# Kernel tuning notes

Hardware: AMD Instinct MI355X
Metric: run time of the kernel (lower is better)

## Reference

```python
import jax, jax.numpy as jnp
import numpy as np

NMS_PRE_MAXSIZE = 4096
NMS_POST_MAXSIZE = 512
NMS_THRESH = 0.7


def setup_inputs() -> dict:
    key = jax.random.key(0)
    k1, k2, k3, k4, k5 = jax.random.split(key, 5)
    B, N, C = 4, 32768, 3
    # realistic 3D boxes: (x, y, z, dx, dy, dz, heading)
    xy = jax.random.uniform(k1, (B, N, 2), dtype=jnp.float32) * 70.0
    z = jax.random.uniform(k2, (B, N, 1), dtype=jnp.float32) * 4.0 - 2.0
    sizes = jax.random.uniform(k3, (B, N, 3), dtype=jnp.float32) * 3.0 + 1.0
    heading = jax.random.uniform(k4, (B, N, 1), dtype=jnp.float32) * 6.2832 - 3.1416
    batch_box_preds = jnp.concatenate([xy, z, sizes, heading], axis=-1)  # (B,N,7)
    batch_cls_preds = jax.random.uniform(k5, (B, N, C), dtype=jnp.float32)  # (B,N,3)
    return {"batch_box_preds": batch_box_preds, "batch_cls_preds": batch_cls_preds}


def _nms_single(boxes, scores, labels):
    # boxes (N,7), scores (N,), labels (N,) int32
    top_s, idx = jax.lax.top_k(scores, NMS_PRE_MAXSIZE)   # sort desc, keep pre-maxsize
    b = boxes[idx]                                        # (PRE,7)
    l = labels[idx]
    # BEV axis-aligned IoU (reference surrogate for the rotated-BEV CUDA IoU kernel)
    x, y, dx, dy = b[:, 0], b[:, 1], b[:, 3], b[:, 4]
    x1, x2 = x - 0.5 * dx, x + 0.5 * dx
    y1, y2 = y - 0.5 * dy, y + 0.5 * dy
    area = dx * dy
    ix = jnp.maximum(0.0, jnp.minimum(x2[:, None], x2[None, :]) - jnp.maximum(x1[:, None], x1[None, :]))
    iy = jnp.maximum(0.0, jnp.minimum(y2[:, None], y2[None, :]) - jnp.maximum(y1[:, None], y1[None, :]))
    inter = ix * iy
    iou = jax.lax.stop_gradient(inter / (area[:, None] + area[None, :] - inter + 1e-6))

    ar = jnp.arange(NMS_PRE_MAXSIZE)

    def body(i, keep):
        sup = (iou[i] > NMS_THRESH) & (ar > i) & keep[i]
        return keep & ~sup

    keep = jax.lax.fori_loop(0, NMS_PRE_MAXSIZE, body, jnp.ones(NMS_PRE_MAXSIZE, bool))

    # pack first NMS_POST_MAXSIZE kept boxes into fixed-size zero-padded outputs
    rank = jnp.cumsum(keep) - 1
    valid = keep & (rank < NMS_POST_MAXSIZE)
    pos = jnp.where(valid, rank, NMS_POST_MAXSIZE)  # invalid -> scratch row
    rois = jnp.zeros((NMS_POST_MAXSIZE + 1, 7), b.dtype).at[pos].set(b)[:NMS_POST_MAXSIZE]
    sc = jnp.zeros((NMS_POST_MAXSIZE + 1,), top_s.dtype).at[pos].set(top_s)[:NMS_POST_MAXSIZE]
    lb = jnp.zeros((NMS_POST_MAXSIZE + 1,), jnp.int32).at[pos].set(l)[:NMS_POST_MAXSIZE]
    return rois, sc, lb


def reference(batch_box_preds, batch_cls_preds):
    # per-box max score / argmax class (torch.max(cls_preds, dim=1) per sample)
    roi_scores_all = jnp.max(batch_cls_preds, axis=-1)                 # (B,N)
    roi_labels_all = jnp.argmax(batch_cls_preds, axis=-1).astype(jnp.int32)
    rois, roi_scores, roi_labels = jax.vmap(_nms_single)(batch_box_preds, roi_scores_all, roi_labels_all)
    return rois, roi_scores, roi_labels + 1  # labels shifted by +1 as in proposal_layer
```

## Files before the change

kernel.cpp:

```cpp
#include <hip/hip_runtime.h>
#include <stdint.h>

#define BB 4
#define NN 32768
#define PRE 4096
#define POST 512
#define NMS_TH 0.7f
#define MIDCAP 8192
#define P1G 16

typedef unsigned long long u64;
typedef unsigned int u32;

__device__ __forceinline__ u32 orderable(float f) {
  u32 u = __float_as_uint(f);
  return (u & 0x80000000u) ? ~u : (u | 0x80000000u);
}
__device__ __forceinline__ float unorderable(u32 o) {
  u32 u = (o & 0x80000000u) ? (o & 0x7fffffffu) : ~o;
  return __uint_as_float(u);
}
__device__ __forceinline__ u32 bucket_of(float s) {
  u32 v = (u32)(s * 2147483648.0f);
  u32 bk = v >> 20;
  return bk > 2047u ? 2047u : bk;
}
__device__ __forceinline__ u64 readlane64(u64 v, int l) {
  u32 lo = (u32)__builtin_amdgcn_readlane((int)(u32)v, l);
  u32 hi = (u32)__builtin_amdgcn_readlane((int)(u32)(v >> 32), l);
  return ((u64)hi << 32) | lo;
}

__global__ void zero_kernel(u32* __restrict__ hist, u32* __restrict__ cnt_mid,
                            u64* __restrict__ rowAnyBm) {
  int t = blockIdx.x * 256 + threadIdx.x;
  if (t < BB * 2048) hist[t] = 0;
  if (t < BB * 64) rowAnyBm[t] = 0;
  if (t < BB) cnt_mid[t] = 0;
}

__global__ __launch_bounds__(256) void score_hist_kernel(const float* __restrict__ cls,
                                                         int* __restrict__ labels,
                                                         u64* __restrict__ keys,
                                                         u32* __restrict__ hist) {
  __shared__ u32 lh[2048];
  for (int t = threadIdx.x; t < 2048; t += 256) lh[t] = 0;
  __syncthreads();
  int g = blockIdx.x * 256 + threadIdx.x;
  const float* c = cls + (size_t)g * 3;
  float s = c[0]; int l = 0;
  float c1 = c[1], c2 = c[2];
  if (c1 > s) { s = c1; l = 1; }
  if (c2 > s) { s = c2; l = 2; }
  int n = g & (NN - 1);
  keys[g] = ((u64)orderable(s) << 32) | (u32)(~(u32)n);
  labels[g] = l;
  atomicAdd(&lh[bucket_of(s)], 1u);
  __syncthreads();
  int b = blockIdx.x >> 7;
  for (int t = threadIdx.x; t < 2048; t += 256) {
    u32 v = lh[t];
    if (v) atomicAdd(&hist[b * 2048 + t], v);
  }
}

__global__ __launch_bounds__(256) void select_kernel(const u32* __restrict__ hist,
                                                     u32* __restrict__ selinfo,
                                                     u32* __restrict__ sfxBuf,
                                                     u32* __restrict__ cursor) {
  __shared__ u32 sfx[2048];
  int b = blockIdx.x;
  for (int t = threadIdx.x; t < 2048; t += 256) sfx[t] = hist[b * 2048 + t];
  __syncthreads();
  for (int d = 1; d < 2048; d <<= 1) {
    u32 v[8];
#pragma unroll
    for (int i = 0; i < 8; ++i) {
      int t = threadIdx.x + i * 256;
      v[i] = (t + d < 2048) ? sfx[t + d] : 0;
    }
    __syncthreads();
#pragma unroll
    for (int i = 0; i < 8; ++i) sfx[threadIdx.x + i * 256] += v[i];
    __syncthreads();
  }
  for (int t = threadIdx.x; t < 2048; t += 256) {
    u32 above = (t + 1 < 2048) ? sfx[t + 1] : 0;
    sfxBuf[b * 2048 + t] = sfx[t];
    cursor[b * 2048 + t] = above;
    if (above < PRE && sfx[t] >= PRE) { selinfo[b * 2] = (u32)t; selinfo[b * 2 + 1] = above; }
  }
}

__global__ __launch_bounds__(256) void compact_kernel(const u64* __restrict__ keys,
                                                      const u32* __restrict__ selinfo,
                                                      u32* __restrict__ cursor,
                                                      u64* __restrict__ sel, u64* __restrict__ mid,
                                                      u32* __restrict__ cnt_mid) {
  int g = blockIdx.x * 256 + threadIdx.x;
  int b = g >> 15;
  u64 key = keys[g];
  u32 bk = bucket_of(unorderable((u32)(key >> 32)));
  u32 T = selinfo[b * 2];
  if (bk > T) {
    u32 p = atomicAdd(&cursor[b * 2048 + bk], 1u);
    sel[((size_t)b << 12) + p] = key;
  } else if (bk == T) {
    u32 p = atomicAdd(&cnt_mid[b], 1u);
    if (p < MIDCAP) mid[(size_t)b * MIDCAP + p] = key;
  }
}

__global__ __launch_bounds__(64) void bsort_kernel(u64* __restrict__ sel, u64* __restrict__ mid,
                                                   const u32* __restrict__ sfxBuf,
                                                   const u32* __restrict__ selinfo,
                                                   const u32* __restrict__ cnt_mid,
                                                   const float* __restrict__ boxes,
                                                   const int* __restrict__ labels,
                                                   float* __restrict__ topBox,
                                                   float4* __restrict__ P,
                                                   float* __restrict__ AR,
                                                   float* __restrict__ topS,
                                                   int* __restrict__ topL) {
  int t = blockIdx.x & 2047;
  int b = blockIdx.x >> 11;
  int lane = threadIdx.x;
  u32 T = selinfo[b * 2];
  if ((u32)t < T) return;
  u64* selB = sel + ((size_t)b << 12);
  u32 start, end;
  if ((u32)t == T) {
    u32 C1 = selinfo[b * 2 + 1];
    int need = PRE - (int)C1;
    int M = (int)cnt_mid[b]; if (M > MIDCAP) M = MIDCAP;
    u64* midB = mid + (size_t)b * MIDCAP;
    for (int r = 0; r < need; ++r) {
      u64 best = 0; int bi = -1;
      for (int q = lane; q < M; q += 64) {
        u64 v = midB[q];
        if (v > best) { best = v; bi = q; }
      }
#pragma unroll
      for (int d = 32; d > 0; d >>= 1) {
        u64 ob = __shfl_xor(best, d, 64);
        int oi = __shfl_xor(bi, d, 64);
        if (ob > best) { best = ob; bi = oi; }
      }
      if (lane == 0) selB[C1 + r] = best;
      if (bi >= 0 && lane == (bi & 63)) midB[bi] = 0;
    }
    start = C1; end = PRE;
  } else {
    start = (t < 2047) ? sfxBuf[b * 2048 + t + 1] : 0u;
    end = sfxBuf[b * 2048 + t];
    int n = (int)(end - start);
    if (n > 64) {
      for (int r = 0; r < n - 1; ++r) {
        u64 best = 0; int bi = -1;
        for (int q = r + lane; q < n; q += 64) {
          u64 v = selB[start + q];
          if (v > best) { best = v; bi = q; }
        }
#pragma unroll
        for (int d = 32; d > 0; d >>= 1) {
          u64 ob = __shfl_xor(best, d, 64);
          int oi = __shfl_xor(bi, d, 64);
          if (ob > best) { best = ob; bi = oi; }
        }
        if (lane == 0) {
          u64 tmp = selB[start + r];
          selB[start + r] = best;
          selB[start + bi] = tmp;
        }
      }
    } else if (n > 1) {
      u64 v = (lane < n) ? selB[start + lane] : 0ULL;
#pragma unroll
      for (int k = 2; k <= 64; k <<= 1) {
#pragma unroll
        for (int j = k >> 1; j > 0; j >>= 1) {
          u64 o = __shfl_xor(v, j, 64);
          bool up = ((lane & k) == 0);
          bool first = ((lane & j) == 0);
          u64 mx = v > o ? v : o, mn = v > o ? o : v;
          v = (first == up) ? mx : mn;
        }
      }
      if (lane < n) selB[start + lane] = v;
    }
  }
  __builtin_amdgcn_s_waitcnt(0);
  for (u32 pos = start + lane; pos < end; pos += 64) {
    u64 key = selB[pos];
    u32 n = ~(u32)key;
    size_t src = (size_t)b * NN + n;
    const float* bx = boxes + src * 7;
    float x = bx[0], y = bx[1], dx = bx[3], dy = bx[4];
    size_t gidx = ((size_t)b << 12) + pos;
    float* tb = topBox + gidx * 7;
#pragma unroll
    for (int c = 0; c < 7; ++c) tb[c] = bx[c];
    float4 p;
    p.x = x - 0.5f * dx; p.z = x + 0.5f * dx;
    p.y = y - 0.5f * dy; p.w = y + 0.5f * dy;
    P[gidx] = p;
    AR[gidx] = dx * dy;
    topS[gidx] = unorderable((u32)(key >> 32));
    topL[gidx] = labels[src];
  }
}

__device__ __forceinline__ void mask_tile(int b, int rb, int w, int lane,
                                          const float4* __restrict__ P,
                                          const float* __restrict__ AR,
                                          u64* __restrict__ maskT,
                                          u64* __restrict__ diag,
                                          u64* __restrict__ rowAnyBm) {
  int base = b << 12;
  int row = (rb << 6) + lane;
  float4 rp = P[base + row];
  float rar = AR[base + row];
  const float4* __restrict__ Pcol = P + base + (w << 6);
  const float* __restrict__ ARcol = AR + base + (w << 6);
  u64 bits = 0;
  float margMin = 1.0f;
#pragma unroll 8
  for (int k = 0; k < 64; ++k) {
    float4 cb = Pcol[k];
    float ca = ARcol[k];
    float ix = fminf(rp.z, cb.z) - fmaxf(rp.x, cb.x); ix = fmaxf(0.0f, ix);
    float iy = fminf(rp.w, cb.w) - fmaxf(rp.y, cb.y); iy = fmaxf(0.0f, iy);
    float inter = ix * iy;
    float denom = ((rar + ca) - inter) + 1e-6f;
    float t = 0.7f * denom;
    bits |= ((u64)(inter > t ? 1u : 0u)) << k;
    margMin = fminf(margMin, fabsf(inter - t) - 2e-5f * t);
  }
  if (__any(margMin <= 0.0f)) {
    bits = 0;
    for (int k = 0; k < 64; ++k) {
      float4 cb = Pcol[k];
      float ca = ARcol[k];
      float ix = fminf(rp.z, cb.z) - fmaxf(rp.x, cb.x); ix = fmaxf(0.0f, ix);
      float iy = fminf(rp.w, cb.w) - fmaxf(rp.y, cb.y); iy = fmaxf(0.0f, iy);
      float inter = ix * iy;
      float denom = ((rar + ca) - inter) + 1e-6f;
      bits |= ((u64)(((inter / denom) > NMS_TH) ? 1u : 0u)) << k;
    }
  }
  maskT[((size_t)(b * 64 + w)) * PRE + row] = bits;
  if (w == rb) diag[base + row] = bits;
  else {
    u64 anyw = __ballot(bits != 0ULL);
    if (lane == 0 && anyw)
      atomicOr((unsigned long long*)&rowAnyBm[b * 64 + rb], anyw);
  }
}

__global__ __launch_bounds__(256) void mask1_kernel(const float4* __restrict__ P,
                                                    const float* __restrict__ AR,
                                                    u64* __restrict__ maskT,
                                                    u64* __restrict__ diag,
                                                    u64* __restrict__ rowAnyBm) {
  int b = blockIdx.y;
  int ti = blockIdx.x * 4 + (threadIdx.x >> 6);
  int lane = threadIdx.x & 63;
  int rb = 0;
  while (rb < P1G - 1 && (64 * (rb + 1) - ((rb + 1) * rb) / 2) <= ti) ++rb;
  int w = rb + (ti - (64 * rb - (rb * (rb - 1)) / 2));
  mask_tile(b, rb, w, lane, P, AR, maskT, diag, rowAnyBm);
}

__global__ __launch_bounds__(256) void mask2_kernel(const float4* __restrict__ P,
                                                    const float* __restrict__ AR,
                                                    u64* __restrict__ maskT,
                                                    u64* __restrict__ diag,
                                                    u64* __restrict__ rowAnyBm,
                                                    const u32* __restrict__ doneFlag) {
  int b = blockIdx.y;
  if (doneFlag[b]) return;
  int ti = blockIdx.x * 4 + (threadIdx.x >> 6);
  int lane = threadIdx.x & 63;
  int rr = 0;
  while (rr < 47 && (48 * (rr + 1) - ((rr + 1) * rr) / 2) <= ti) ++rr;
  int rb = rr + P1G;
  int w = rb + (ti - (48 * rr - (rr * (rr - 1)) / 2));
  mask_tile(b, rb, w, lane, P, AR, maskT, diag, rowAnyBm);
}

__global__ __launch_bounds__(64, 1) void scan_kernel(const u64* __restrict__ maskT,
                                                     const u64* __restrict__ diag,
                                                     const u64* __restrict__ rowAnyBm,
                                                     const float* __restrict__ topBox,
                                                     const float* __restrict__ topS,
                                                     const int* __restrict__ topL,
                                                     float* __restrict__ out,
                                                     u64* __restrict__ rState,
                                                     u64* __restrict__ kwState,
                                                     u32* __restrict__ nkState,
                                                     u32* __restrict__ doneFlag,
                                                     int phase) {
  __shared__ u64 kwLDS[64];
  __shared__ u64 dgLDS[3072];
  int b = blockIdx.x;
  int lane = threadIdx.x;
  if (phase == 1 && doneFlag[b]) return;
  const u64* m = maskT + (size_t)b * 64 * PRE;
  const u64* dg = diag + (size_t)b * PRE;
  u64 rowAnyW = rowAnyBm[b * 64 + lane];
  u64 r; int nk, gs, ge;
  if (phase == 0) {
    kwLDS[lane] = 0; r = 0; nk = 0; gs = 0; ge = P1G;
  } else {
    kwLDS[lane] = (lane < P1G) ? kwState[b * 64 + lane] : 0;
    r = rState[b * 64 + lane]; nk = nkState[b]; gs = P1G; ge = 64;
  }
  for (int t = lane; t < (ge - gs) * 64; t += 64) dgLDS[t] = dg[(size_t)gs * 64 + t];
  __syncthreads();
  bool done = false;
  for (int g = gs; g < ge; ++g) {
    u64 d_cur = dgLDS[(g - gs) * 64 + lane];
    u64 aboveMask = ~((2ULL << lane) - 1ULL);
    u64 rem = __ballot((d_cur & aboveMask) != 0ULL);
    u64 sup = readlane64(r, g);
    if (rem) {
      do {
        int k = __ffsll((long long)rem) - 1;
        rem &= rem - 1;
        if (!((sup >> k) & 1ULL))
          sup |= readlane64(d_cur, k) & ~((2ULL << k) - 1ULL);
      } while (rem);
    }
    u64 keep = ~sup;
    u64 need = keep & readlane64(rowAnyW, g);
    if (need) {
      u64 accr = 0;
      do {
        int t = __ffsll((long long)need) - 1;
        need &= need - 1;
        accr |= m[(size_t)lane * PRE + (size_t)(g << 6) + t];
      } while (need);
      r |= accr;
    }
    if (lane == 0) kwLDS[g] = keep;
    nk += (int)__popcll(keep);
    if (nk >= POST) { done = true; break; }
  }
  __syncthreads();
  if (phase == 0 && !done) {
    rState[b * 64 + lane] = r;
    if (lane < P1G) kwState[b * 64 + lane] = kwLDS[lane];
    if (lane == 0) { nkState[b] = nk; doneFlag[b] = 0; }
    return;
  }
  if (phase == 0 && lane == 0) doneFlag[b] = 1;
  u64 kw = kwLDS[lane];
  int cnt = __popcll(kw);
  int pfx = cnt;
#pragma unroll
  for (int d = 1; d < 64; d <<= 1) {
    int up = __shfl_up(pfx, d, 64);
    if (lane >= d) pfx += up;
  }
  int total = __shfl(pfx, 63, 64);
  int pos = pfx - cnt;
  float* outR = out;
  float* outS = out + BB * POST * 7;
  float* outL = outS + BB * POST;
  while (kw) {
    int t = __ffsll((long long)kw) - 1;
    kw &= kw - 1;
    if (pos < POST) {
      int i = (lane << 6) + t;
      int g = (b << 9) + pos;
      const float* tb = topBox + ((size_t)(b << 12) + i) * 7;
#pragma unroll
      for (int c = 0; c < 7; ++c) outR[(size_t)g * 7 + c] = tb[c];
      outS[g] = topS[(b << 12) + i];
      outL[g] = (float)(topL[(b << 12) + i] + 1);
    }
    ++pos;
  }
  int fin = total < POST ? total : POST;
  for (int s = fin + lane; s < POST; s += 64) {
    int g = (b << 9) + s;
#pragma unroll
    for (int c = 0; c < 7; ++c) outR[(size_t)g * 7 + c] = 0.0f;
    outS[g] = 0.0f;
    outL[g] = 1.0f;
  }
}

extern "C" void kernel_launch(void* const* d_in, const int* in_sizes, int n_in,
                              void* d_out, int out_size, void* d_ws, size_t ws_size,
                              hipStream_t stream) {
  const float* boxes = (const float*)d_in[0];
  const float* cls   = (const float*)d_in[1];
  float* out = (float*)d_out;

  char* p = (char*)d_ws;
  auto take = [&](size_t bytes) { char* r = p; p += (bytes + 255) & ~(size_t)255; return (void*)r; };
  u64*   keys    = (u64*)  take((size_t)BB * NN * 8);
  int*   labels  = (int*)  take((size_t)BB * NN * 4);
  u32*   hist    = (u32*)  take((size_t)BB * 2048 * 4);
  u32*   selinfo = (u32*)  take((size_t)BB * 2 * 4);
  u32*   sfxBuf  = (u32*)  take((size_t)BB * 2048 * 4);
  u32*   cursor  = (u32*)  take((size_t)BB * 2048 * 4);
  u32*   cnt_mid = (u32*)  take((size_t)BB * 4);
  u64*   sel     = (u64*)  take((size_t)BB * PRE * 8);
  u64*   mid     = (u64*)  take((size_t)BB * MIDCAP * 8);
  float* topBox  = (float*)take((size_t)BB * PRE * 7 * 4);
  float4* Pb     = (float4*)take((size_t)BB * PRE * 16);
  float* AR      = (float*)take((size_t)BB * PRE * 4);
  float* topS    = (float*)take((size_t)BB * PRE * 4);
  int*   topL    = (int*)  take((size_t)BB * PRE * 4);
  u64*   maskT   = (u64*)  take((size_t)BB * 64 * PRE * 8);
  u64*   diagBuf = (u64*)  take((size_t)BB * PRE * 8);
  u64*   rowAny  = (u64*)  take((size_t)BB * 64 * 8);
  u64*   rState  = (u64*)  take((size_t)BB * 64 * 8);
  u64*   kwState = (u64*)  take((size_t)BB * 64 * 8);
  u32*   nkState = (u32*)  take((size_t)BB * 4);
  u32*   doneFlg = (u32*)  take((size_t)BB * 4);

  zero_kernel<<<32, 256, 0, stream>>>(hist, cnt_mid, rowAny);
  score_hist_kernel<<<BB * NN / 256, 256, 0, stream>>>(cls, labels, keys, hist);
  select_kernel<<<BB, 256, 0, stream>>>(hist, selinfo, sfxBuf, cursor);
  compact_kernel<<<BB * NN / 256, 256, 0, stream>>>(keys, selinfo, cursor, sel, mid, cnt_mid);
  bsort_kernel<<<BB * 2048, 64, 0, stream>>>(sel, mid, sfxBuf, selinfo, cnt_mid,
                                             boxes, labels, topBox, Pb, AR, topS, topL);
  mask1_kernel<<<dim3(226, BB), 256, 0, stream>>>(Pb, AR, maskT, diagBuf, rowAny);
  scan_kernel<<<BB, 64, 0, stream>>>(maskT, diagBuf, rowAny, topBox, topS, topL, out,
                                     rState, kwState, nkState, doneFlg, 0);
  mask2_kernel<<<dim3(294, BB), 256, 0, stream>>>(Pb, AR, maskT, diagBuf, rowAny, doneFlg);
  scan_kernel<<<BB, 64, 0, stream>>>(maskT, diagBuf, rowAny, topBox, topS, topL, out,
                                     rState, kwState, nkState, doneFlg, 1);
}
```

Measured before the change: 91.16 us.

## Vectorize score/compact kernels four items per thread and shrink phase-1 NMS mask region

The score-histogram and compact kernels now handle four boxes per thread, using float4 and 128-bit loads and stores, and launch a quarter as many blocks. The first NMS phase now computes mask tiles for only the first 10 row-groups instead of 16, with tile counts and the mask2 index mapping generalized to match. The aim is to cut memory-transaction overhead in the streaming kernels and reduce mask work done before the early-exit scan. The trade-off is that when 512 boxes are not kept within the first 640 candidates, more mask work falls to the second phase.

New measurement: 85.90 us. 5.8% less time.

```diff
diff --git a/kernel.cpp b/kernel.cpp
--- a/kernel.cpp
+++ b/kernel.cpp
@@ -7,7 +7,9 @@
 #define POST 512
 #define NMS_TH 0.7f
 #define MIDCAP 8192
-#define P1G 16
+#define P1G 10
+#define T1 595
+#define T2 1485
 
 typedef unsigned long long u64;
 typedef unsigned int u32;
@@ -46,21 +48,30 @@
   __shared__ u32 lh[2048];
   for (int t = threadIdx.x; t < 2048; t += 256) lh[t] = 0;
   __syncthreads();
-  int g = blockIdx.x * 256 + threadIdx.x;
-  const float* c = cls + (size_t)g * 3;
-  float s = c[0]; int l = 0;
-  float c1 = c[1], c2 = c[2];
-  if (c1 > s) { s = c1; l = 1; }
-  if (c2 > s) { s = c2; l = 2; }
-  int n = g & (NN - 1);
-  keys[g] = ((u64)orderable(s) << 32) | (u32)(~(u32)n);
-  labels[g] = l;
-  atomicAdd(&lh[bucket_of(s)], 1u);
+  int t4 = blockIdx.x * 256 + threadIdx.x;
+  int base4 = t4 * 4;
+  const float4* c4 = (const float4*)(cls + (size_t)t4 * 12);
+  float4 va = c4[0], vb = c4[1], vc = c4[2];
+  float v[12] = {va.x, va.y, va.z, va.w, vb.x, vb.y, vb.z, vb.w, vc.x, vc.y, vc.z, vc.w};
+  u64 ks[4]; int ls[4];
+#pragma unroll
+  for (int p = 0; p < 4; ++p) {
+    float s = v[3 * p]; int l = 0;
+    if (v[3 * p + 1] > s) { s = v[3 * p + 1]; l = 1; }
+    if (v[3 * p + 2] > s) { s = v[3 * p + 2]; l = 2; }
+    int n = (base4 + p) & (NN - 1);
+    ks[p] = ((u64)orderable(s) << 32) | (u32)(~(u32)n);
+    ls[p] = l;
+    atomicAdd(&lh[bucket_of(s)], 1u);
+  }
+  *(ulonglong2*)(keys + base4) = make_ulonglong2(ks[0], ks[1]);
+  *(ulonglong2*)(keys + base4 + 2) = make_ulonglong2(ks[2], ks[3]);
+  *(int4*)(labels + base4) = make_int4(ls[0], ls[1], ls[2], ls[3]);
   __syncthreads();
-  int b = blockIdx.x >> 7;
+  int b = blockIdx.x >> 5;
   for (int t = threadIdx.x; t < 2048; t += 256) {
-    u32 v = lh[t];
-    if (v) atomicAdd(&hist[b * 2048 + t], v);
+    u32 vv = lh[t];
+    if (vv) atomicAdd(&hist[b * 2048 + t], vv);
   }
 }
 
@@ -97,17 +108,24 @@
                                                       u32* __restrict__ cursor,
                                                       u64* __restrict__ sel, u64* __restrict__ mid,
                                                       u32* __restrict__ cnt_mid) {
-  int g = blockIdx.x * 256 + threadIdx.x;
-  int b = g >> 15;
-  u64 key = keys[g];
-  u32 bk = bucket_of(unorderable((u32)(key >> 32)));
+  int t4 = blockIdx.x * 256 + threadIdx.x;
+  int base4 = t4 * 4;
+  int b = base4 >> 15;
   u32 T = selinfo[b * 2];
-  if (bk > T) {
-    u32 p = atomicAdd(&cursor[b * 2048 + bk], 1u);
-    sel[((size_t)b << 12) + p] = key;
-  } else if (bk == T) {
-    u32 p = atomicAdd(&cnt_mid[b], 1u);
-    if (p < MIDCAP) mid[(size_t)b * MIDCAP + p] = key;
+  ulonglong2 k01 = *(const ulonglong2*)(keys + base4);
+  ulonglong2 k23 = *(const ulonglong2*)(keys + base4 + 2);
+  u64 kk[4] = {k01.x, k01.y, k23.x, k23.y};
+#pragma unroll
+  for (int p = 0; p < 4; ++p) {
+    u64 key = kk[p];
+    u32 bk = bucket_of(unorderable((u32)(key >> 32)));
+    if (bk > T) {
+      u32 q = atomicAdd(&cursor[b * 2048 + bk], 1u);
+      sel[((size_t)b << 12) + q] = key;
+    } else if (bk == T) {
+      u32 q = atomicAdd(&cnt_mid[b], 1u);
+      if (q < MIDCAP) mid[(size_t)b * MIDCAP + q] = key;
+    }
   }
 }
 
@@ -264,6 +282,7 @@
                                                     u64* __restrict__ rowAnyBm) {
   int b = blockIdx.y;
   int ti = blockIdx.x * 4 + (threadIdx.x >> 6);
+  if (ti >= T1) return;
   int lane = threadIdx.x & 63;
   int rb = 0;
   while (rb < P1G - 1 && (64 * (rb + 1) - ((rb + 1) * rb) / 2) <= ti) ++rb;
@@ -280,11 +299,13 @@
   int b = blockIdx.y;
   if (doneFlag[b]) return;
   int ti = blockIdx.x * 4 + (threadIdx.x >> 6);
+  if (ti >= T2) return;
   int lane = threadIdx.x & 63;
+  int R = 64 - P1G;
   int rr = 0;
-  while (rr < 47 && (48 * (rr + 1) - ((rr + 1) * rr) / 2) <= ti) ++rr;
+  while (rr < R - 1 && (R * (rr + 1) - ((rr + 1) * rr) / 2) <= ti) ++rr;
   int rb = rr + P1G;
-  int w = rb + (ti - (48 * rr - (rr * (rr - 1)) / 2));
+  int w = rb + (ti - (R * rr - (rr * (rr - 1)) / 2));
   mask_tile(b, rb, w, lane, P, AR, maskT, diag, rowAnyBm);
 }
 
@@ -301,7 +322,7 @@
                                                      u32* __restrict__ doneFlag,
                                                      int phase) {
   __shared__ u64 kwLDS[64];
-  __shared__ u64 dgLDS[3072];
+  __shared__ u64 dgLDS[(64 - P1G) * 64];
   int b = blockIdx.x;
   int lane = threadIdx.x;
   if (phase == 1 && doneFlag[b]) return;
@@ -423,15 +444,15 @@
   u32*   doneFlg = (u32*)  take((size_t)BB * 4);
 
   zero_kernel<<<32, 256, 0, stream>>>(hist, cnt_mid, rowAny);
-  score_hist_kernel<<<BB * NN / 256, 256, 0, stream>>>(cls, labels, keys, hist);
+  score_hist_kernel<<<BB * NN / 1024, 256, 0, stream>>>(cls, labels, keys, hist);
   select_kernel<<<BB, 256, 0, stream>>>(hist, selinfo, sfxBuf, cursor);
-  compact_kernel<<<BB * NN / 256, 256, 0, stream>>>(keys, selinfo, cursor, sel, mid, cnt_mid);
+  compact_kernel<<<BB * NN / 1024, 256, 0, stream>>>(keys, selinfo, cursor, sel, mid, cnt_mid);
   bsort_kernel<<<BB * 2048, 64, 0, stream>>>(sel, mid, sfxBuf, selinfo, cnt_mid,
                                              boxes, labels, topBox, Pb, AR, topS, topL);
-  mask1_kernel<<<dim3(226, BB), 256, 0, stream>>>(Pb, AR, maskT, diagBuf, rowAny);
+  mask1_kernel<<<dim3((T1 + 3) / 4, BB), 256, 0, stream>>>(Pb, AR, maskT, diagBuf, rowAny);
   scan_kernel<<<BB, 64, 0, stream>>>(maskT, diagBuf, rowAny, topBox, topS, topL, out,
                                      rState, kwState, nkState, doneFlg, 0);
-  mask2_kernel<<<dim3(294, BB), 256, 0, stream>>>(Pb, AR, maskT, diagBuf, rowAny, doneFlg);
+  mask2_kernel<<<dim3((T2 + 3) / 4, BB), 256, 0, stream>>>(Pb, AR, maskT, diagBuf, rowAny, doneFlg);
   scan_kernel<<<BB, 64, 0, stream>>>(maskT, diagBuf, rowAny, topBox, topS, topL, out,
                                      rState, kwState, nkState, doneFlg, 1);
 }
```
